# Performance work log

Hardware: AMD Instinct MI355X
Metric: run time of the kernel (lower is better)

The kernel has to match this reference:

```python
import jax, jax.numpy as jnp
import numpy as np

B, N, M, D = 4096, 50, 64, 64   # batch, fields_dim, embedding_dim, product_layer_dim
V = 100000                      # features_dim (vocab)
HIDDEN = [512, 256, 128]
BN_EPS = 1e-3


def setup_inputs() -> dict:
    key = jax.random.key(0)
    ks = jax.random.split(key, 32)
    inp = {
        "feature_value": jax.random.uniform(ks[0], (B, N), dtype=jnp.float32),
        "embedding_index": jax.random.randint(ks[1], (B, N), 0, V, dtype=jnp.int32),
        "emb_table": jax.random.uniform(ks[2], (V, M), dtype=jnp.float32, minval=-0.05, maxval=0.05),
        "linear_signals": jax.random.normal(ks[3], (D, N, M), dtype=jnp.float32) * 0.05,
        "theta": jax.random.normal(ks[4], (D, N), dtype=jnp.float32) * 0.05,
        "quad_w": jax.random.normal(ks[5], (D, M, M), dtype=jnp.float32) * 0.05,
    }
    in_dim = 3 * D  # concat(l_z, l_p_inner, l_p_outer)
    dims = [in_dim] + HIDDEN
    k = 6
    for i, (di, do) in enumerate(zip(dims[:-1], dims[1:])):
        inp[f"W{i}"] = jax.random.normal(ks[k], (di, do), dtype=jnp.float32) * (1.0 / np.sqrt(di)); k += 1
        inp[f"b{i}"] = jnp.zeros((do,), dtype=jnp.float32)
        inp[f"g{i}"] = jnp.ones((do,), dtype=jnp.float32)
        inp[f"be{i}"] = jnp.zeros((do,), dtype=jnp.float32)
        inp[f"m{i}"] = jnp.zeros((do,), dtype=jnp.float32)
        inp[f"v{i}"] = jnp.ones((do,), dtype=jnp.float32)
    inp["Wout"] = jax.random.normal(ks[k], (HIDDEN[-1], 1), dtype=jnp.float32) * (1.0 / np.sqrt(HIDDEN[-1]))
    inp["bout"] = jnp.zeros((1,), dtype=jnp.float32)
    return inp


def _pnn_forward(feature_value, embedding_index, emb_table, linear_signals, theta, quad_w,
                 dense_params, Wout, bout):
    # features: [b, n, m] = embedding lookup scaled per-field by feature_value
    feats = emb_table[embedding_index] * feature_value[:, :, None]
    # linear signal: 'bnm,dnm->bd'
    l_z = jnp.einsum('bnm,dnm->bd', feats, linear_signals)
    # ipnn branch: delta = 'dn,bnm->bdnm'; l_p = sum delta*delta over (n,m)
    # algebraic rewrite (same math): sum_n theta_dn^2 * (sum_m feats_bnm^2)
    l_p_in = jnp.einsum('bn,dn->bd', jnp.sum(feats * feats, axis=2), theta * theta)
    # opnn branch: p = outer(sum_feats, sum_feats); 'bmn,dmn->bd'
    s = jnp.sum(feats, axis=1)  # [b, m]
    l_p_out = jnp.einsum('bm,dmn,bn->bd', s, quad_w, s)
    x = jnp.concatenate([l_z, l_p_in, l_p_out], axis=1)  # [b, 3d]
    # MLP stack: Dense -> BatchNorm(inference) -> ReLU (dropout is identity at eval)
    for (W, b, g, be, mu, var) in dense_params:
        x = x @ W + b
        x = g * (x - mu) * jax.lax.rsqrt(var + BN_EPS) + be
        x = jax.nn.relu(x)
    return jax.nn.sigmoid(x @ Wout + bout)


def reference(feature_value, embedding_index, emb_table, linear_signals, theta, quad_w,
              W0, b0, g0, be0, m0, v0,
              W1, b1, g1, be1, m1, v1,
              W2, b2, g2, be2, m2, v2,
              Wout, bout):
    dense_params = [(W0, b0, g0, be0, m0, v0),
                    (W1, b1, g1, be1, m1, v1),
                    (W2, b2, g2, be2, m2, v2)]
    return _pnn_forward(feature_value, embedding_index, emb_table, linear_signals, theta,
                        quad_w, dense_params, Wout, bout)
```

## Files before the change

### kernel.cpp

```cpp
#include <hip/hip_runtime.h>
#include <hip/hip_bf16.h>
#include <math.h>

#define B 4096
#define NF 50
#define BN_EPS 1e-3f
#define ROWS 16

typedef float f32x4 __attribute__((ext_vector_type(4)));
typedef __bf16 bf16x8 __attribute__((ext_vector_type(8)));

__device__ __forceinline__ unsigned short f2b(float x) {
  unsigned u = __float_as_uint(x);
  return (unsigned short)((u + 0x7FFFu + ((u >> 16) & 1u)) >> 16);
}
__device__ __forceinline__ float bs2f(unsigned short u) {
  return __uint_as_float(((unsigned)u) << 16);
}
__device__ __forceinline__ unsigned packbf(float a, float b) {
  return ((unsigned)f2b(b) << 16) | (unsigned)f2b(a);
}

#define WS_LS  0
#define WS_QW  204800
#define WS_W0  466944
#define WS_W1  565248
#define WS_W2  696320
#define WS_TOT 729088

__global__ __launch_bounds__(256) void prep(
    const float* __restrict__ ls, const float* __restrict__ qw,
    const float* __restrict__ W0, const float* __restrict__ W1,
    const float* __restrict__ W2, unsigned short* __restrict__ ws)
{
  int o = blockIdx.x * 256 + threadIdx.x;
  if (o < 204800) { ws[WS_LS + o] = f2b(ls[o]); return; }
  o -= 204800;
  if (o < 262144) { ws[WS_QW + o] = f2b(qw[o]); return; }
  o -= 262144;
  if (o < 98304) { int n = o / 192, k = o - n * 192; ws[WS_W0 + o] = f2b(W0[k * 512 + n]); return; }
  o -= 98304;
  if (o < 131072) { int n = o >> 9, k = o & 511; ws[WS_W1 + o] = f2b(W1[k * 256 + n]); return; }
  o -= 131072;
  if (o < 32768) { int n = o >> 8, k = o & 255; ws[WS_W2 + o] = f2b(W2[k * 128 + n]); }
}

#define BIG_SHORTS 41216

__global__ __launch_bounds__(512) void pnn_main(
    const float* __restrict__ fv, const int* __restrict__ idx,
    const float* __restrict__ emb, const float* __restrict__ theta,
    const unsigned short* __restrict__ ws,
    const float* __restrict__ b0p, const float* __restrict__ g0p,
    const float* __restrict__ be0p, const float* __restrict__ m0p,
    const float* __restrict__ v0p,
    const float* __restrict__ b1p, const float* __restrict__ g1p,
    const float* __restrict__ be1p, const float* __restrict__ m1p,
    const float* __restrict__ v1p,
    const float* __restrict__ b2p, const float* __restrict__ g2p,
    const float* __restrict__ be2p, const float* __restrict__ m2p,
    const float* __restrict__ v2p,
    const float* __restrict__ Wout, const float* __restrict__ boutp,
    float* __restrict__ out)
{
  __shared__ int   idx_s[ROWS * NF];
  __shared__ float fv_s[ROWS * NF];
  __shared__ float th2_s[64 * NF];
  __shared__ float s_s[ROWS * 64];
  __shared__ float sq_s[ROWS * 64];
  __shared__ unsigned short x_s[ROWS * 200];
  __shared__ float red_s[4 * 256];
  __shared__ unsigned short h0_s[ROWS * 520];
  __shared__ unsigned short big[BIG_SHORTS];

  unsigned short* ls_lo = big;
  unsigned short* ls_hi = big + 8704;
  unsigned short* f_lo  = big + 17408;
  unsigned short* f_hi  = big + 19584;
  unsigned short* h1_s  = big + 34816;
  unsigned short* h2_s  = big + 39040;

  const unsigned short* lsb = ws + WS_LS;
  const unsigned short* qwb = ws + WS_QW;
  const unsigned short* w0t = ws + WS_W0;
  const unsigned short* w1t = ws + WS_W1;
  const unsigned short* w2t = ws + WS_W2;

  const int t  = threadIdx.x;
  const int w  = t >> 6;
  const int l  = t & 63;
  const int b0 = blockIdx.x * ROWS;
  const int bq = t >> 5;
  const int i2 = (t & 31) * 2;

  for (int i = t; i < ROWS * NF; i += 512) { idx_s[i] = idx[b0 * NF + i]; fv_s[i] = fv[b0 * NF + i]; }
  for (int i = t; i < 64 * NF; i += 512) { float v = theta[i]; th2_s[i] = v * v; }
  __syncthreads();

  float s0 = 0.f, s1 = 0.f;
  f32x4 az0 = {0.f, 0.f, 0.f, 0.f};
  f32x4 az1 = {0.f, 0.f, 0.f, 0.f};
  const int kh = w >> 2;
  const int d0 = (w & 3) * 16;
  const int arow = (l & 15) * 136 + (l >> 4) * 8;

  for (int c = 0; c < 13; ++c) {
#pragma unroll
    for (int h = 0; h < 4; ++h) {
      int n = 4 * c + h;
      if (n < NF) {
        int iv = idx_s[bq * NF + n];
        float fvv = fv_s[bq * NF + n];
        float2 e = *(const float2*)(emb + (size_t)iv * 64 + i2);
        float p0 = fvv * e.x, p1 = fvv * e.y;
        unsigned short* dst = (h < 2) ? f_lo : f_hi;
        *(unsigned*)&dst[bq * 136 + (h & 1) * 64 + i2] = packbf(p0, p1);
        s0 += p0; s1 += p1;
        float q = p0 * p0 + p1 * p1;
        q += __shfl_xor(q, 16); q += __shfl_xor(q, 8); q += __shfl_xor(q, 4);
        q += __shfl_xor(q, 2);  q += __shfl_xor(q, 1);
        if ((t & 31) == 0) sq_s[bq * 64 + n] = q;
      }
    }
    {
      int dd = t >> 3, p = t & 7;
      if (c < 12 || p < 4) {
        const unsigned short* src = lsb + dd * 3200 + 256 * c + p * 32;
        unsigned short* drow = ((p < 4) ? ls_lo : ls_hi) + dd * 136 + (p & 3) * 32;
#pragma unroll
        for (int j = 0; j < 4; ++j)
          *(int4*)&drow[j * 8] = *(const int4*)&src[j * 8];
      }
    }
    __syncthreads();
    if (!(kh == 1 && c == 12)) {
      const unsigned short* ft = kh ? f_hi : f_lo;
      const unsigned short* lt = kh ? ls_hi : ls_lo;
      int brow = (d0 + (l & 15)) * 136 + (l >> 4) * 8;
      bf16x8 a0 = *(const bf16x8*)&ft[arow];
      bf16x8 a1 = *(const bf16x8*)&ft[arow + 32];
      bf16x8 a2 = *(const bf16x8*)&ft[arow + 64];
      bf16x8 a3 = *(const bf16x8*)&ft[arow + 96];
      bf16x8 v0 = *(const bf16x8*)&lt[brow];
      bf16x8 v1 = *(const bf16x8*)&lt[brow + 32];
      bf16x8 v2 = *(const bf16x8*)&lt[brow + 64];
      bf16x8 v3 = *(const bf16x8*)&lt[brow + 96];
      az0 = __builtin_amdgcn_mfma_f32_16x16x32_bf16(a0, v0, az0, 0, 0, 0);
      az1 = __builtin_amdgcn_mfma_f32_16x16x32_bf16(a1, v1, az1, 0, 0, 0);
      az0 = __builtin_amdgcn_mfma_f32_16x16x32_bf16(a2, v2, az0, 0, 0, 0);
      az1 = __builtin_amdgcn_mfma_f32_16x16x32_bf16(a3, v3, az1, 0, 0, 0);
    }
    __syncthreads();
  }
  { float2 sv; sv.x = s0; sv.y = s1; *(float2*)&s_s[bq * 64 + i2] = sv; }
  __syncthreads();

  {
    f32x4 cz;
#pragma unroll
    for (int r = 0; r < 4; ++r) cz[r] = az0[r] + az1[r];
    if (w >= 4) {
      int base = (w - 4) * 256;
#pragma unroll
      for (int r = 0; r < 4; ++r)
        red_s[base + ((l >> 4) * 4 + r) * 16 + (l & 15)] = cz[r];
    }
    __syncthreads();
    if (w < 4) {
      int base = w * 256;
#pragma unroll
      for (int r = 0; r < 4; ++r) {
        float v = cz[r] + red_s[base + ((l >> 4) * 4 + r) * 16 + (l & 15)];
        x_s[((l >> 4) * 4 + r) * 200 + w * 16 + (l & 15)] = f2b(v);
      }
    }
    int d = t & 63, g = t >> 6;
#pragma unroll
    for (int e = 0; e < 2; ++e) {
      int b = g + 8 * e;
      float a = 0.f;
      for (int n = 0; n < NF; ++n) a += sq_s[b * 64 + n] * th2_s[d * NF + n];
      x_s[b * 200 + 64 + d] = f2b(a);
    }
  }
  __syncthreads();

  {
    f32x4 ap0 = {0.f, 0.f, 0.f, 0.f};
    f32x4 ap1 = {0.f, 0.f, 0.f, 0.f};
    for (int c = 0; c < 16; ++c) {
#pragma unroll
      for (int h = 0; h < 4; ++h) {
        int m = 4 * c + h;
        float pm = s_s[bq * 64 + m];
        float p0 = pm * s_s[bq * 64 + i2];
        float p1 = pm * s_s[bq * 64 + i2 + 1];
        unsigned short* dst = (h < 2) ? f_lo : f_hi;
        *(unsigned*)&dst[bq * 136 + (h & 1) * 64 + i2] = packbf(p0, p1);
      }
      {
        int dd = t >> 3, p = t & 7;
        const unsigned short* src = qwb + dd * 4096 + 256 * c + p * 32;
        unsigned short* drow = ((p < 4) ? ls_lo : ls_hi) + dd * 136 + (p & 3) * 32;
#pragma unroll
        for (int j = 0; j < 4; ++j)
          *(int4*)&drow[j * 8] = *(const int4*)&src[j * 8];
      }
      __syncthreads();
      {
        const unsigned short* ft = kh ? f_hi : f_lo;
        const unsigned short* qt = kh ? ls_hi : ls_lo;
        int brow = (d0 + (l & 15)) * 136 + (l >> 4) * 8;
        bf16x8 a0 = *(const bf16x8*)&ft[arow];
        bf16x8 a1 = *(const bf16x8*)&ft[arow + 32];
        bf16x8 a2 = *(const bf16x8*)&ft[arow + 64];
        bf16x8 a3 = *(const bf16x8*)&ft[arow + 96];
        bf16x8 v0 = *(const bf16x8*)&qt[brow];
        bf16x8 v1 = *(const bf16x8*)&qt[brow + 32];
        bf16x8 v2 = *(const bf16x8*)&qt[brow + 64];
        bf16x8 v3 = *(const bf16x8*)&qt[brow + 96];
        ap0 = __builtin_amdgcn_mfma_f32_16x16x32_bf16(a0, v0, ap0, 0, 0, 0);
        ap1 = __builtin_amdgcn_mfma_f32_16x16x32_bf16(a1, v1, ap1, 0, 0, 0);
        ap0 = __builtin_amdgcn_mfma_f32_16x16x32_bf16(a2, v2, ap0, 0, 0, 0);
        ap1 = __builtin_amdgcn_mfma_f32_16x16x32_bf16(a3, v3, ap1, 0, 0, 0);
      }
      __syncthreads();
    }
    f32x4 cp;
#pragma unroll
    for (int r = 0; r < 4; ++r) cp[r] = ap0[r] + ap1[r];
    if (w >= 4) {
      int base = (w - 4) * 256;
#pragma unroll
      for (int r = 0; r < 4; ++r)
        red_s[base + ((l >> 4) * 4 + r) * 16 + (l & 15)] = cp[r];
    }
    __syncthreads();
    if (w < 4) {
      int base = w * 256;
#pragma unroll
      for (int r = 0; r < 4; ++r) {
        float v = cp[r] + red_s[base + ((l >> 4) * 4 + r) * 16 + (l & 15)];
        x_s[((l >> 4) * 4 + r) * 200 + 128 + w * 16 + (l & 15)] = f2b(v);
      }
    }
  }
  __syncthreads();

  unsigned short* wb = big + w * 4352;

  for (int j = 0; j < 4; ++j) {
    int n0 = (w * 4 + j) * 16;
    const unsigned short* src = w0t + n0 * 192;
#pragma unroll
    for (int q = 0; q < 6; ++q) {
      int o = (l + 64 * q) * 8;
      int nn = o / 192, kk = o - nn * 192;
      *(int4*)&wb[nn * 200 + kk] = *(const int4*)&src[o];
    }
    f32x4 ha = {0.f, 0.f, 0.f, 0.f}, hb = {0.f, 0.f, 0.f, 0.f};
    int ar = (l & 15) * 200 + (l >> 4) * 8;
#pragma unroll
    for (int kk = 0; kk < 6; ++kk) {
      bf16x8 av = *(const bf16x8*)&x_s[ar + kk * 32];
      bf16x8 bv = *(const bf16x8*)&wb[ar + kk * 32];
      if (kk & 1) hb = __builtin_amdgcn_mfma_f32_16x16x32_bf16(av, bv, hb, 0, 0, 0);
      else        ha = __builtin_amdgcn_mfma_f32_16x16x32_bf16(av, bv, ha, 0, 0, 0);
    }
    int n = n0 + (l & 15);
    float sc = g0p[n] * rsqrtf(v0p[n] + BN_EPS);
    float sh = be0p[n] + (b0p[n] - m0p[n]) * sc;
#pragma unroll
    for (int r = 0; r < 4; ++r) {
      float v = fmaxf((ha[r] + hb[r]) * sc + sh, 0.f);
      h0_s[((l >> 4) * 4 + r) * 520 + n] = f2b(v);
    }
  }
  __syncthreads();

  for (int j = 0; j < 2; ++j) {
    int n0 = (w * 2 + j) * 16;
    f32x4 ha = {0.f, 0.f, 0.f, 0.f}, hb = {0.f, 0.f, 0.f, 0.f};
    for (int kc = 0; kc < 4; ++kc) {
      unsigned short* cb = wb + (kc & 1) * 2176;
      const unsigned short* src = w1t + n0 * 512 + kc * 128;
#pragma unroll
      for (int q = 0; q < 4; ++q) {
        int o = (l + 64 * q) * 8;
        int nn = o >> 7, kk = o & 127;
        *(int4*)&cb[nn * 136 + kk] = *(const int4*)&src[nn * 512 + kk];
      }
      int ar = (l & 15) * 520 + kc * 128 + (l >> 4) * 8;
      int br = (l & 15) * 136 + (l >> 4) * 8;
#pragma unroll
      for (int kk = 0; kk < 4; ++kk) {
        bf16x8 av = *(const bf16x8*)&h0_s[ar + kk * 32];
        bf16x8 bv = *(const bf16x8*)&cb[br + kk * 32];
        if (kk & 1) hb = __builtin_amdgcn_mfma_f32_16x16x32_bf16(av, bv, hb, 0, 0, 0);
        else        ha = __builtin_amdgcn_mfma_f32_16x16x32_bf16(av, bv, ha, 0, 0, 0);
      }
    }
    int n = n0 + (l & 15);
    float sc = g1p[n] * rsqrtf(v1p[n] + BN_EPS);
    float sh = be1p[n] + (b1p[n] - m1p[n]) * sc;
#pragma unroll
    for (int r = 0; r < 4; ++r) {
      float v = fmaxf((ha[r] + hb[r]) * sc + sh, 0.f);
      h1_s[((l >> 4) * 4 + r) * 264 + n] = f2b(v);
    }
  }
  __syncthreads();

  {
    int n0 = w * 16;
    f32x4 ha = {0.f, 0.f, 0.f, 0.f}, hb = {0.f, 0.f, 0.f, 0.f};
    for (int kc = 0; kc < 2; ++kc) {
      unsigned short* cb = wb + (kc & 1) * 2176;
      const unsigned short* src = w2t + n0 * 256 + kc * 128;
#pragma unroll
      for (int q = 0; q < 4; ++q) {
        int o = (l + 64 * q) * 8;
        int nn = o >> 7, kk = o & 127;
        *(int4*)&cb[nn * 136 + kk] = *(const int4*)&src[nn * 256 + kk];
      }
      int ar = (l & 15) * 264 + kc * 128 + (l >> 4) * 8;
      int br = (l & 15) * 136 + (l >> 4) * 8;
#pragma unroll
      for (int kk = 0; kk < 4; ++kk) {
        bf16x8 av = *(const bf16x8*)&h1_s[ar + kk * 32];
        bf16x8 bv = *(const bf16x8*)&cb[br + kk * 32];
        if (kk & 1) hb = __builtin_amdgcn_mfma_f32_16x16x32_bf16(av, bv, hb, 0, 0, 0);
        else        ha = __builtin_amdgcn_mfma_f32_16x16x32_bf16(av, bv, ha, 0, 0, 0);
      }
    }
    int n = n0 + (l & 15);
    float sc = g2p[n] * rsqrtf(v2p[n] + BN_EPS);
    float sh = be2p[n] + (b2p[n] - m2p[n]) * sc;
#pragma unroll
    for (int r = 0; r < 4; ++r) {
      float v = fmaxf((ha[r] + hb[r]) * sc + sh, 0.f);
      h2_s[((l >> 4) * 4 + r) * 136 + n] = f2b(v);
    }
  }
  __syncthreads();

  if (t < 128) {
    int b = t >> 3, seg = t & 7;
    float a = 0.f;
#pragma unroll
    for (int j = 0; j < 16; ++j) {
      int k = seg * 16 + j;
      a += bs2f(h2_s[b * 136 + k]) * Wout[k];
    }
    a += __shfl_xor(a, 4); a += __shfl_xor(a, 2); a += __shfl_xor(a, 1);
    if (seg == 0) out[b0 + b] = 1.f / (1.f + expf(-(a + boutp[0])));
  }
}

extern "C" void kernel_launch(void* const* d_in, const int* in_sizes, int n_in,
                              void* d_out, int out_size, void* d_ws, size_t ws_size,
                              hipStream_t stream)
{
  (void)in_sizes; (void)n_in; (void)out_size; (void)ws_size;
  const float* fv   = (const float*)d_in[0];
  const int*   idx  = (const int*)d_in[1];
  const float* emb  = (const float*)d_in[2];
  const float* ls   = (const float*)d_in[3];
  const float* th   = (const float*)d_in[4];
  const float* qw   = (const float*)d_in[5];
  unsigned short* ws = (unsigned short*)d_ws;

  prep<<<(WS_TOT + 255) / 256, 256, 0, stream>>>(
      ls, qw, (const float*)d_in[6], (const float*)d_in[12],
      (const float*)d_in[18], ws);

  pnn_main<<<B / ROWS, 512, 0, stream>>>(
      fv, idx, emb, th, ws,
      (const float*)d_in[7],  (const float*)d_in[8],  (const float*)d_in[9],
      (const float*)d_in[10], (const float*)d_in[11],
      (const float*)d_in[13], (const float*)d_in[14], (const float*)d_in[15],
      (const float*)d_in[16], (const float*)d_in[17],
      (const float*)d_in[19], (const float*)d_in[20], (const float*)d_in[21],
      (const float*)d_in[22], (const float*)d_in[23],
      (const float*)d_in[24], (const float*)d_in[25],
      (float*)d_out);
}
```

Measured before the change: 183.8 us.

## Read weights directly from global into MFMA operands, shrink LDS, vectorize prep

Result: slower. 207.5 us (+12.9%).

```diff
diff --git a/kernel.cpp b/kernel.cpp
--- a/kernel.cpp
+++ b/kernel.cpp
@@ -9,16 +9,17 @@
 
 typedef float f32x4 __attribute__((ext_vector_type(4)));
 typedef __bf16 bf16x8 __attribute__((ext_vector_type(8)));
+#define MFMA __builtin_amdgcn_mfma_f32_16x16x32_bf16
 
 __device__ __forceinline__ unsigned short f2b(float x) {
   unsigned u = __float_as_uint(x);
   return (unsigned short)((u + 0x7FFFu + ((u >> 16) & 1u)) >> 16);
 }
+__device__ __forceinline__ unsigned packbf(float a, float b) {
+  return ((unsigned)f2b(b) << 16) | (unsigned)f2b(a);
+}
 __device__ __forceinline__ float bs2f(unsigned short u) {
   return __uint_as_float(((unsigned)u) << 16);
-}
-__device__ __forceinline__ unsigned packbf(float a, float b) {
-  return ((unsigned)f2b(b) << 16) | (unsigned)f2b(a);
 }
 
 #define WS_LS  0
@@ -26,28 +27,61 @@
 #define WS_W0  466944
 #define WS_W1  565248
 #define WS_W2  696320
-#define WS_TOT 729088
 
 __global__ __launch_bounds__(256) void prep(
     const float* __restrict__ ls, const float* __restrict__ qw,
     const float* __restrict__ W0, const float* __restrict__ W1,
     const float* __restrict__ W2, unsigned short* __restrict__ ws)
 {
-  int o = blockIdx.x * 256 + threadIdx.x;
-  if (o < 204800) { ws[WS_LS + o] = f2b(ls[o]); return; }
-  o -= 204800;
-  if (o < 262144) { ws[WS_QW + o] = f2b(qw[o]); return; }
-  o -= 262144;
-  if (o < 98304) { int n = o / 192, k = o - n * 192; ws[WS_W0 + o] = f2b(W0[k * 512 + n]); return; }
-  o -= 98304;
-  if (o < 131072) { int n = o >> 9, k = o & 511; ws[WS_W1 + o] = f2b(W1[k * 256 + n]); return; }
-  o -= 131072;
-  if (o < 32768) { int n = o >> 8, k = o & 255; ws[WS_W2 + o] = f2b(W2[k * 128 + n]); }
-}
-
-#define BIG_SHORTS 41216
-
-__global__ __launch_bounds__(512) void pnn_main(
+  int tid = blockIdx.x * 256 + threadIdx.x;
+  if (tid < 25600) {
+    int o = tid * 8;
+    float4 a = *(const float4*)(ls + o), b = *(const float4*)(ls + o + 4);
+    int4 v = {(int)packbf(a.x, a.y), (int)packbf(a.z, a.w),
+              (int)packbf(b.x, b.y), (int)packbf(b.z, b.w)};
+    *(int4*)&ws[WS_LS + o] = v; return;
+  }
+  tid -= 25600;
+  if (tid < 32768) {
+    int o = tid * 8;
+    float4 a = *(const float4*)(qw + o), b = *(const float4*)(qw + o + 4);
+    int4 v = {(int)packbf(a.x, a.y), (int)packbf(a.z, a.w),
+              (int)packbf(b.x, b.y), (int)packbf(b.z, b.w)};
+    *(int4*)&ws[WS_QW + o] = v; return;
+  }
+  tid -= 32768;
+  if (tid < 12288) {
+    int n = tid / 24, k0 = (tid - n * 24) * 8;
+    float f[8];
+#pragma unroll
+    for (int j = 0; j < 8; ++j) f[j] = W0[(k0 + j) * 512 + n];
+    int4 v = {(int)packbf(f[0], f[1]), (int)packbf(f[2], f[3]),
+              (int)packbf(f[4], f[5]), (int)packbf(f[6], f[7])};
+    *(int4*)&ws[WS_W0 + n * 192 + k0] = v; return;
+  }
+  tid -= 12288;
+  if (tid < 16384) {
+    int n = tid >> 6, k0 = (tid & 63) * 8;
+    float f[8];
+#pragma unroll
+    for (int j = 0; j < 8; ++j) f[j] = W1[(k0 + j) * 256 + n];
+    int4 v = {(int)packbf(f[0], f[1]), (int)packbf(f[2], f[3]),
+              (int)packbf(f[4], f[5]), (int)packbf(f[6], f[7])};
+    *(int4*)&ws[WS_W1 + n * 512 + k0] = v; return;
+  }
+  tid -= 16384;
+  if (tid < 4096) {
+    int n = tid >> 5, k0 = (tid & 31) * 8;
+    float f[8];
+#pragma unroll
+    for (int j = 0; j < 8; ++j) f[j] = W2[(k0 + j) * 128 + n];
+    int4 v = {(int)packbf(f[0], f[1]), (int)packbf(f[2], f[3]),
+              (int)packbf(f[4], f[5]), (int)packbf(f[6], f[7])};
+    *(int4*)&ws[WS_W2 + n * 256 + k0] = v;
+  }
+}
+
+__global__ __launch_bounds__(512, 4) void pnn_main(
     const float* __restrict__ fv, const int* __restrict__ idx,
     const float* __restrict__ emb, const float* __restrict__ theta,
     const unsigned short* __restrict__ ws,
@@ -65,20 +99,14 @@
 {
   __shared__ int   idx_s[ROWS * NF];
   __shared__ float fv_s[ROWS * NF];
-  __shared__ float th2_s[64 * NF];
   __shared__ float s_s[ROWS * 64];
   __shared__ float sq_s[ROWS * 64];
+  __shared__ float red_s[4 * 256];
   __shared__ unsigned short x_s[ROWS * 200];
-  __shared__ float red_s[4 * 256];
   __shared__ unsigned short h0_s[ROWS * 520];
-  __shared__ unsigned short big[BIG_SHORTS];
-
-  unsigned short* ls_lo = big;
-  unsigned short* ls_hi = big + 8704;
-  unsigned short* f_lo  = big + 17408;
-  unsigned short* f_hi  = big + 19584;
-  unsigned short* h1_s  = big + 34816;
-  unsigned short* h2_s  = big + 39040;
+  __shared__ unsigned short h1_s[ROWS * 264];
+  __shared__ unsigned short h2_s[ROWS * 136];
+  __shared__ unsigned short fbuf[2 * 2 * ROWS * 136];
 
   const unsigned short* lsb = ws + WS_LS;
   const unsigned short* qwb = ws + WS_QW;
@@ -89,22 +117,25 @@
   const int t  = threadIdx.x;
   const int w  = t >> 6;
   const int l  = t & 63;
+  const int m16 = l & 15;
+  const int qoff = (l >> 4) * 8;
   const int b0 = blockIdx.x * ROWS;
   const int bq = t >> 5;
   const int i2 = (t & 31) * 2;
-
-  for (int i = t; i < ROWS * NF; i += 512) { idx_s[i] = idx[b0 * NF + i]; fv_s[i] = fv[b0 * NF + i]; }
-  for (int i = t; i < 64 * NF; i += 512) { float v = theta[i]; th2_s[i] = v * v; }
-  __syncthreads();
-
-  float s0 = 0.f, s1 = 0.f;
-  f32x4 az0 = {0.f, 0.f, 0.f, 0.f};
-  f32x4 az1 = {0.f, 0.f, 0.f, 0.f};
   const int kh = w >> 2;
   const int d0 = (w & 3) * 16;
-  const int arow = (l & 15) * 136 + (l >> 4) * 8;
+
+  for (int i = t; i < ROWS * NF; i += 512) {
+    idx_s[i] = idx[b0 * NF + i];
+    fv_s[i]  = fv[b0 * NF + i];
+  }
+  __syncthreads();
+
+  float s0 = 0.f, s1 = 0.f;
+  f32x4 az0 = {0.f, 0.f, 0.f, 0.f}, az1 = {0.f, 0.f, 0.f, 0.f};
 
   for (int c = 0; c < 13; ++c) {
+    unsigned short* fb = fbuf + (c & 1) * 4352;
 #pragma unroll
     for (int h = 0; h < 4; ++h) {
       int n = 4 * c + h;
@@ -113,8 +144,7 @@
         float fvv = fv_s[bq * NF + n];
         float2 e = *(const float2*)(emb + (size_t)iv * 64 + i2);
         float p0 = fvv * e.x, p1 = fvv * e.y;
-        unsigned short* dst = (h < 2) ? f_lo : f_hi;
-        *(unsigned*)&dst[bq * 136 + (h & 1) * 64 + i2] = packbf(p0, p1);
+        *(unsigned*)&fb[(h >> 1) * 2176 + bq * 136 + (h & 1) * 64 + i2] = packbf(p0, p1);
         s0 += p0; s1 += p1;
         float q = p0 * p0 + p1 * p1;
         q += __shfl_xor(q, 16); q += __shfl_xor(q, 8); q += __shfl_xor(q, 4);
@@ -122,35 +152,24 @@
         if ((t & 31) == 0) sq_s[bq * 64 + n] = q;
       }
     }
-    {
-      int dd = t >> 3, p = t & 7;
-      if (c < 12 || p < 4) {
-        const unsigned short* src = lsb + dd * 3200 + 256 * c + p * 32;
-        unsigned short* drow = ((p < 4) ? ls_lo : ls_hi) + dd * 136 + (p & 3) * 32;
-#pragma unroll
-        for (int j = 0; j < 4; ++j)
-          *(int4*)&drow[j * 8] = *(const int4*)&src[j * 8];
-      }
-    }
     __syncthreads();
     if (!(kh == 1 && c == 12)) {
-      const unsigned short* ft = kh ? f_hi : f_lo;
-      const unsigned short* lt = kh ? ls_hi : ls_lo;
-      int brow = (d0 + (l & 15)) * 136 + (l >> 4) * 8;
-      bf16x8 a0 = *(const bf16x8*)&ft[arow];
-      bf16x8 a1 = *(const bf16x8*)&ft[arow + 32];
-      bf16x8 a2 = *(const bf16x8*)&ft[arow + 64];
-      bf16x8 a3 = *(const bf16x8*)&ft[arow + 96];
-      bf16x8 v0 = *(const bf16x8*)&lt[brow];
-      bf16x8 v1 = *(const bf16x8*)&lt[brow + 32];
-      bf16x8 v2 = *(const bf16x8*)&lt[brow + 64];
-      bf16x8 v3 = *(const bf16x8*)&lt[brow + 96];
-      az0 = __builtin_amdgcn_mfma_f32_16x16x32_bf16(a0, v0, az0, 0, 0, 0);
-      az1 = __builtin_amdgcn_mfma_f32_16x16x32_bf16(a1, v1, az1, 0, 0, 0);
-      az0 = __builtin_amdgcn_mfma_f32_16x16x32_bf16(a2, v2, az0, 0, 0, 0);
-      az1 = __builtin_amdgcn_mfma_f32_16x16x32_bf16(a3, v3, az1, 0, 0, 0);
-    }
-    __syncthreads();
+      const unsigned short* fa = fb + kh * 2176;
+      const unsigned short* lp = lsb + (d0 + m16) * 3200 + 256 * c + kh * 128 + qoff;
+      int ar = m16 * 136 + qoff;
+      bf16x8 bv0 = *(const bf16x8*)(lp);
+      bf16x8 bv1 = *(const bf16x8*)(lp + 32);
+      bf16x8 bv2 = *(const bf16x8*)(lp + 64);
+      bf16x8 bv3 = *(const bf16x8*)(lp + 96);
+      bf16x8 a0 = *(const bf16x8*)&fa[ar];
+      bf16x8 a1 = *(const bf16x8*)&fa[ar + 32];
+      bf16x8 a2 = *(const bf16x8*)&fa[ar + 64];
+      bf16x8 a3 = *(const bf16x8*)&fa[ar + 96];
+      az0 = MFMA(a0, bv0, az0, 0, 0, 0);
+      az1 = MFMA(a1, bv1, az1, 0, 0, 0);
+      az0 = MFMA(a2, bv2, az0, 0, 0, 0);
+      az1 = MFMA(a3, bv3, az1, 0, 0, 0);
+    }
   }
   { float2 sv; sv.x = s0; sv.y = s1; *(float2*)&s_s[bq * 64 + i2] = sv; }
   __syncthreads();
@@ -163,144 +182,124 @@
       int base = (w - 4) * 256;
 #pragma unroll
       for (int r = 0; r < 4; ++r)
-        red_s[base + ((l >> 4) * 4 + r) * 16 + (l & 15)] = cz[r];
+        red_s[base + ((l >> 4) * 4 + r) * 16 + m16] = cz[r];
     }
     __syncthreads();
     if (w < 4) {
       int base = w * 256;
 #pragma unroll
       for (int r = 0; r < 4; ++r) {
-        float v = cz[r] + red_s[base + ((l >> 4) * 4 + r) * 16 + (l & 15)];
-        x_s[((l >> 4) * 4 + r) * 200 + w * 16 + (l & 15)] = f2b(v);
+        float v = cz[r] + red_s[base + ((l >> 4) * 4 + r) * 16 + m16];
+        x_s[((l >> 4) * 4 + r) * 200 + w * 16 + m16] = f2b(v);
       }
     }
     int d = t & 63, g = t >> 6;
 #pragma unroll
     for (int e = 0; e < 2; ++e) {
-      int b = g + 8 * e;
+      int bb = g + 8 * e;
       float a = 0.f;
-      for (int n = 0; n < NF; ++n) a += sq_s[b * 64 + n] * th2_s[d * NF + n];
-      x_s[b * 200 + 64 + d] = f2b(a);
+      for (int n = 0; n < NF; ++n) {
+        float th = theta[d * NF + n];
+        a += sq_s[bb * 64 + n] * (th * th);
+      }
+      x_s[bb * 200 + 64 + d] = f2b(a);
     }
   }
   __syncthreads();
 
   {
-    f32x4 ap0 = {0.f, 0.f, 0.f, 0.f};
-    f32x4 ap1 = {0.f, 0.f, 0.f, 0.f};
+    f32x4 ap0 = {0.f, 0.f, 0.f, 0.f}, ap1 = {0.f, 0.f, 0.f, 0.f};
     for (int c = 0; c < 16; ++c) {
+      unsigned short* fb = fbuf + (c & 1) * 4352;
 #pragma unroll
       for (int h = 0; h < 4; ++h) {
-        int m = 4 * c + h;
-        float pm = s_s[bq * 64 + m];
+        int mq = 4 * c + h;
+        float pm = s_s[bq * 64 + mq];
         float p0 = pm * s_s[bq * 64 + i2];
         float p1 = pm * s_s[bq * 64 + i2 + 1];
-        unsigned short* dst = (h < 2) ? f_lo : f_hi;
-        *(unsigned*)&dst[bq * 136 + (h & 1) * 64 + i2] = packbf(p0, p1);
-      }
-      {
-        int dd = t >> 3, p = t & 7;
-        const unsigned short* src = qwb + dd * 4096 + 256 * c + p * 32;
-        unsigned short* drow = ((p < 4) ? ls_lo : ls_hi) + dd * 136 + (p & 3) * 32;
-#pragma unroll
-        for (int j = 0; j < 4; ++j)
-          *(int4*)&drow[j * 8] = *(const int4*)&src[j * 8];
+        *(unsigned*)&fb[(h >> 1) * 2176 + bq * 136 + (h & 1) * 64 + i2] = packbf(p0, p1);
       }
       __syncthreads();
       {
-        const unsigned short* ft = kh ? f_hi : f_lo;
-        const unsigned short* qt = kh ? ls_hi : ls_lo;
-        int brow = (d0 + (l & 15)) * 136 + (l >> 4) * 8;
-        bf16x8 a0 = *(const bf16x8*)&ft[arow];
-        bf16x8 a1 = *(const bf16x8*)&ft[arow + 32];
-        bf16x8 a2 = *(const bf16x8*)&ft[arow + 64];
-        bf16x8 a3 = *(const bf16x8*)&ft[arow + 96];
-        bf16x8 v0 = *(const bf16x8*)&qt[brow];
-        bf16x8 v1 = *(const bf16x8*)&qt[brow + 32];
-        bf16x8 v2 = *(const bf16x8*)&qt[brow + 64];
-        bf16x8 v3 = *(const bf16x8*)&qt[brow + 96];
-        ap0 = __builtin_amdgcn_mfma_f32_16x16x32_bf16(a0, v0, ap0, 0, 0, 0);
-        ap1 = __builtin_amdgcn_mfma_f32_16x16x32_bf16(a1, v1, ap1, 0, 0, 0);
-        ap0 = __builtin_amdgcn_mfma_f32_16x16x32_bf16(a2, v2, ap0, 0, 0, 0);
-        ap1 = __builtin_amdgcn_mfma_f32_16x16x32_bf16(a3, v3, ap1, 0, 0, 0);
-      }
-      __syncthreads();
+        const unsigned short* fa = fb + kh * 2176;
+        const unsigned short* qp = qwb + (d0 + m16) * 4096 + 256 * c + kh * 128 + qoff;
+        int ar = m16 * 136 + qoff;
+        bf16x8 bv0 = *(const bf16x8*)(qp);
+        bf16x8 bv1 = *(const bf16x8*)(qp + 32);
+        bf16x8 bv2 = *(const bf16x8*)(qp + 64);
+        bf16x8 bv3 = *(const bf16x8*)(qp + 96);
+        bf16x8 a0 = *(const bf16x8*)&fa[ar];
+        bf16x8 a1 = *(const bf16x8*)&fa[ar + 32];
+        bf16x8 a2 = *(const bf16x8*)&fa[ar + 64];
+        bf16x8 a3 = *(const bf16x8*)&fa[ar + 96];
+        ap0 = MFMA(a0, bv0, ap0, 0, 0, 0);
+        ap1 = MFMA(a1, bv1, ap1, 0, 0, 0);
+        ap0 = MFMA(a2, bv2, ap0, 0, 0, 0);
+        ap1 = MFMA(a3, bv3, ap1, 0, 0, 0);
+      }
     }
     f32x4 cp;
 #pragma unroll
     for (int r = 0; r < 4; ++r) cp[r] = ap0[r] + ap1[r];
+    __syncthreads();
     if (w >= 4) {
       int base = (w - 4) * 256;
 #pragma unroll
       for (int r = 0; r < 4; ++r)
-        red_s[base + ((l >> 4) * 4 + r) * 16 + (l & 15)] = cp[r];
+        red_s[base + ((l >> 4) * 4 + r) * 16 + m16] = cp[r];
     }
     __syncthreads();
     if (w < 4) {
       int base = w * 256;
 #pragma unroll
       for (int r = 0; r < 4; ++r) {
-        float v = cp[r] + red_s[base + ((l >> 4) * 4 + r) * 16 + (l & 15)];
-        x_s[((l >> 4) * 4 + r) * 200 + 128 + w * 16 + (l & 15)] = f2b(v);
-      }
-    }
-  }
-  __syncthreads();
-
-  unsigned short* wb = big + w * 4352;
-
-  for (int j = 0; j < 4; ++j) {
-    int n0 = (w * 4 + j) * 16;
-    const unsigned short* src = w0t + n0 * 192;
-#pragma unroll
-    for (int q = 0; q < 6; ++q) {
-      int o = (l + 64 * q) * 8;
-      int nn = o / 192, kk = o - nn * 192;
-      *(int4*)&wb[nn * 200 + kk] = *(const int4*)&src[o];
-    }
-    f32x4 ha = {0.f, 0.f, 0.f, 0.f}, hb = {0.f, 0.f, 0.f, 0.f};
-    int ar = (l & 15) * 200 + (l >> 4) * 8;
-#pragma unroll
-    for (int kk = 0; kk < 6; ++kk) {
-      bf16x8 av = *(const bf16x8*)&x_s[ar + kk * 32];
-      bf16x8 bv = *(const bf16x8*)&wb[ar + kk * 32];
-      if (kk & 1) hb = __builtin_amdgcn_mfma_f32_16x16x32_bf16(av, bv, hb, 0, 0, 0);
-      else        ha = __builtin_amdgcn_mfma_f32_16x16x32_bf16(av, bv, ha, 0, 0, 0);
-    }
-    int n = n0 + (l & 15);
-    float sc = g0p[n] * rsqrtf(v0p[n] + BN_EPS);
-    float sh = be0p[n] + (b0p[n] - m0p[n]) * sc;
-#pragma unroll
-    for (int r = 0; r < 4; ++r) {
-      float v = fmaxf((ha[r] + hb[r]) * sc + sh, 0.f);
-      h0_s[((l >> 4) * 4 + r) * 520 + n] = f2b(v);
+        float v = cp[r] + red_s[base + ((l >> 4) * 4 + r) * 16 + m16];
+        x_s[((l >> 4) * 4 + r) * 200 + 128 + w * 16 + m16] = f2b(v);
+      }
+    }
+  }
+  __syncthreads();
+
+  {
+    int ar = m16 * 200 + qoff;
+    bf16x8 xa[6];
+#pragma unroll
+    for (int kc = 0; kc < 6; ++kc) xa[kc] = *(const bf16x8*)&x_s[ar + kc * 32];
+    for (int j = 0; j < 4; ++j) {
+      int n0 = (w * 4 + j) * 16;
+      const unsigned short* wp = w0t + (n0 + m16) * 192 + qoff;
+      f32x4 ha = {0.f, 0.f, 0.f, 0.f}, hb = {0.f, 0.f, 0.f, 0.f};
+#pragma unroll
+      for (int kc = 0; kc < 6; ++kc) {
+        bf16x8 bv = *(const bf16x8*)(wp + kc * 32);
+        if (kc & 1) hb = MFMA(xa[kc], bv, hb, 0, 0, 0);
+        else        ha = MFMA(xa[kc], bv, ha, 0, 0, 0);
+      }
+      int n = n0 + m16;
+      float sc = g0p[n] * rsqrtf(v0p[n] + BN_EPS);
+      float sh = be0p[n] + (b0p[n] - m0p[n]) * sc;
+#pragma unroll
+      for (int r = 0; r < 4; ++r) {
+        float v = fmaxf((ha[r] + hb[r]) * sc + sh, 0.f);
+        h0_s[((l >> 4) * 4 + r) * 520 + n] = f2b(v);
+      }
     }
   }
   __syncthreads();
 
   for (int j = 0; j < 2; ++j) {
     int n0 = (w * 2 + j) * 16;
+    const unsigned short* wp = w1t + (n0 + m16) * 512 + qoff;
+    int ar = m16 * 520 + qoff;
     f32x4 ha = {0.f, 0.f, 0.f, 0.f}, hb = {0.f, 0.f, 0.f, 0.f};
-    for (int kc = 0; kc < 4; ++kc) {
-      unsigned short* cb = wb + (kc & 1) * 2176;
-      const unsigned short* src = w1t + n0 * 512 + kc * 128;
-#pragma unroll
-      for (int q = 0; q < 4; ++q) {
-        int o = (l + 64 * q) * 8;
-        int nn = o >> 7, kk = o & 127;
-        *(int4*)&cb[nn * 136 + kk] = *(const int4*)&src[nn * 512 + kk];
-      }
-      int ar = (l & 15) * 520 + kc * 128 + (l >> 4) * 8;
-      int br = (l & 15) * 136 + (l >> 4) * 8;
-#pragma unroll
-      for (int kk = 0; kk < 4; ++kk) {
-        bf16x8 av = *(const bf16x8*)&h0_s[ar + kk * 32];
-        bf16x8 bv = *(const bf16x8*)&cb[br + kk * 32];
-        if (kk & 1) hb = __builtin_amdgcn_mfma_f32_16x16x32_bf16(av, bv, hb, 0, 0, 0);
-        else        ha = __builtin_amdgcn_mfma_f32_16x16x32_bf16(av, bv, ha, 0, 0, 0);
-      }
-    }
-    int n = n0 + (l & 15);
+#pragma unroll
+    for (int kc = 0; kc < 16; ++kc) {
+      bf16x8 av = *(const bf16x8*)&h0_s[ar + kc * 32];
+      bf16x8 bv = *(const bf16x8*)(wp + kc * 32);
+      if (kc & 1) hb = MFMA(av, bv, hb, 0, 0, 0);
+      else        ha = MFMA(av, bv, ha, 0, 0, 0);
+    }
+    int n = n0 + m16;
     float sc = g1p[n] * rsqrtf(v1p[n] + BN_EPS);
     float sh = be1p[n] + (b1p[n] - m1p[n]) * sc;
 #pragma unroll
@@ -313,27 +312,17 @@
 
   {
     int n0 = w * 16;
+    const unsigned short* wp = w2t + (n0 + m16) * 256 + qoff;
+    int ar = m16 * 264 + qoff;
     f32x4 ha = {0.f, 0.f, 0.f, 0.f}, hb = {0.f, 0.f, 0.f, 0.f};
-    for (int kc = 0; kc < 2; ++kc) {
-      unsigned short* cb = wb + (kc & 1) * 2176;
-      const unsigned short* src = w2t + n0 * 256 + kc * 128;
-#pragma unroll
-      for (int q = 0; q < 4; ++q) {
-        int o = (l + 64 * q) * 8;
-        int nn = o >> 7, kk = o & 127;
-        *(int4*)&cb[nn * 136 + kk] = *(const int4*)&src[nn * 256 + kk];
-      }
-      int ar = (l & 15) * 264 + kc * 128 + (l >> 4) * 8;
-      int br = (l & 15) * 136 + (l >> 4) * 8;
-#pragma unroll
-      for (int kk = 0; kk < 4; ++kk) {
-        bf16x8 av = *(const bf16x8*)&h1_s[ar + kk * 32];
-        bf16x8 bv = *(const bf16x8*)&cb[br + kk * 32];
-        if (kk & 1) hb = __builtin_amdgcn_mfma_f32_16x16x32_bf16(av, bv, hb, 0, 0, 0);
-        else        ha = __builtin_amdgcn_mfma_f32_16x16x32_bf16(av, bv, ha, 0, 0, 0);
-      }
-    }
-    int n = n0 + (l & 15);
+#pragma unroll
+    for (int kc = 0; kc < 8; ++kc) {
+      bf16x8 av = *(const bf16x8*)&h1_s[ar + kc * 32];
+      bf16x8 bv = *(const bf16x8*)(wp + kc * 32);
+      if (kc & 1) hb = MFMA(av, bv, hb, 0, 0, 0);
+      else        ha = MFMA(av, bv, ha, 0, 0, 0);
+    }
+    int n = n0 + m16;
     float sc = g2p[n] * rsqrtf(v2p[n] + BN_EPS);
     float sh = be2p[n] + (b2p[n] - m2p[n]) * sc;
 #pragma unroll
@@ -345,15 +334,15 @@
   __syncthreads();
 
   if (t < 128) {
-    int b = t >> 3, seg = t & 7;
+    int bb = t >> 3, seg = t & 7;
     float a = 0.f;
 #pragma unroll
     for (int j = 0; j < 16; ++j) {
       int k = seg * 16 + j;
-      a += bs2f(h2_s[b * 136 + k]) * Wout[k];
+      a += bs2f(h2_s[bb * 136 + k]) * Wout[k];
     }
     a += __shfl_xor(a, 4); a += __shfl_xor(a, 2); a += __shfl_xor(a, 1);
-    if (seg == 0) out[b0 + b] = 1.f / (1.f + expf(-(a + boutp[0])));
+    if (seg == 0) out[b0 + bb] = 1.f / (1.f + expf(-(a + boutp[0])));
   }
 }
 
@@ -362,20 +351,15 @@
                               hipStream_t stream)
 {
   (void)in_sizes; (void)n_in; (void)out_size; (void)ws_size;
-  const float* fv   = (const float*)d_in[0];
-  const int*   idx  = (const int*)d_in[1];
-  const float* emb  = (const float*)d_in[2];
-  const float* ls   = (const float*)d_in[3];
-  const float* th   = (const float*)d_in[4];
-  const float* qw   = (const float*)d_in[5];
   unsigned short* ws = (unsigned short*)d_ws;
 
-  prep<<<(WS_TOT + 255) / 256, 256, 0, stream>>>(
-      ls, qw, (const float*)d_in[6], (const float*)d_in[12],
-      (const float*)d_in[18], ws);
+  prep<<<356, 256, 0, stream>>>(
+      (const float*)d_in[3], (const float*)d_in[5], (const float*)d_in[6],
+      (const float*)d_in[12], (const float*)d_in[18], ws);
 
   pnn_main<<<B / ROWS, 512, 0, stream>>>(
-      fv, idx, emb, th, ws,
+      (const float*)d_in[0], (const int*)d_in[1], (const float*)d_in[2],
+      (const float*)d_in[4], ws,
       (const float*)d_in[7],  (const float*)d_in[8],  (const float*)d_in[9],
       (const float*)d_in[10], (const float*)d_in[11],
       (const float*)d_in[13], (const float*)d_in[14], (const float*)d_in[15],
```
